# Optimization experiments

Measured on AMD Instinct MI355X. Metric: run time of the kernel, lower is better.

## Reference

```python
import jax, jax.numpy as jnp
import numpy as np

C, IN, OUT = 1024, 256, 256
B, N = 256, 1024

def setup_inputs() -> dict:
    key = jax.random.key(0)
    k1, k2, k3 = jax.random.split(key, 3)
    x = jax.random.normal(k1, (B, N, IN), dtype=jnp.float32)
    indices = jax.random.randint(k2, (B,), 0, C, dtype=jnp.int64)
    # kaiming-uniform-style init for weight table [C, IN, OUT]
    bound = float(np.sqrt(6.0 / IN))
    weight = jax.random.uniform(k3, (C, IN, OUT), dtype=jnp.float32, minval=-bound, maxval=bound)
    bias = jnp.zeros((C, 1, OUT), dtype=jnp.float32)
    return {"x": x, "indices": indices, "weight": weight, "bias": bias}

def reference(x, indices, weight, bias):
    # gather per-batch weight tiles, then batched matmul + bias
    w = weight[indices]          # [B, IN, OUT]
    b = bias[indices]            # [B, 1, OUT]
    return jnp.einsum('bni,bio->bno', x, w) + b
```

## Files before the change

kernel.cpp:

```cpp
#include <hip/hip_runtime.h>
#include <cstdint>

#define C_   1024
#define IN_  256
#define OUT_ 256
#define B_   256
#define N_   1024

#define BM 128
#define BK 32
#define NTHREADS 512

typedef __attribute__((ext_vector_type(8))) short short8;
typedef __attribute__((ext_vector_type(4))) float f32x4;

__device__ __forceinline__ uint16_t f2bf(float f) {
    uint32_t u = __builtin_bit_cast(uint32_t, f);
    return (uint16_t)((u + 0x7FFFu + ((u >> 16) & 1u)) >> 16);
}

__device__ __forceinline__ void glds16(const void* g, void* l) {
    __builtin_amdgcn_global_load_lds(
        (const __attribute__((address_space(1))) void*)g,
        (__attribute__((address_space(3))) void*)l,
        16, 0, 0);
}

__global__ __launch_bounds__(256) void prep_wt(
    const float* __restrict__ weight, const int* __restrict__ idx,
    uint16_t* __restrict__ wt) {
    __shared__ float tile[IN_][33];
    const int b  = blockIdx.y;
    const int o0 = blockIdx.x * 32;
    const int ci = idx[b];
    const float* wsrc = weight + (size_t)ci * (IN_ * OUT_);
    const int t = threadIdx.x;

    const int o_l   = t & 31;
    const int kbase = t >> 5;
    #pragma unroll
    for (int rep = 0; rep < 32; ++rep) {
        int k = rep * 8 + kbase;
        tile[k][o_l] = wsrc[k * OUT_ + o0 + o_l];
    }
    __syncthreads();

    const int k2   = (t & 127) * 2;
    const int osel = t >> 7;
    uint32_t* dst = (uint32_t*)(wt + (size_t)b * (IN_ * OUT_));
    #pragma unroll
    for (int rep = 0; rep < 16; ++rep) {
        int o = rep * 2 + osel;
        uint32_t lo = f2bf(tile[k2][o]);
        uint32_t hi = f2bf(tile[k2 + 1][o]);
        dst[((o0 + o) * IN_ + k2) >> 1] = lo | (hi << 16);
    }
}

__global__ __launch_bounds__(NTHREADS, 2) void gemm_bn256(
    const float* __restrict__ x, const int* __restrict__ idx,
    const uint16_t* __restrict__ wt, const float* __restrict__ bias,
    float* __restrict__ out) {
    __shared__ __align__(16) uint8_t smem[32768];
    uint16_t* As = (uint16_t*)smem;
    uint16_t* Ws = (uint16_t*)(smem + 8192);
    float*    Ep = (float*)smem;

    const int b    = blockIdx.y;
    const int n0   = blockIdx.x * BM;
    const int t    = threadIdx.x;
    const int lane = t & 63;
    const int wv   = t >> 6;
    const int wm   = wv >> 2;
    const int wn   = wv & 3;
    const int m    = lane & 15;
    const int g    = lane >> 4;

    const float*    xsrc = x  + (size_t)b * (N_ * IN_) + (size_t)n0 * IN_;
    const uint16_t* wsrc = wt + (size_t)b * (IN_ * OUT_);

    const int arow = t >> 2, aq = t & 3;
    const float* aptr = xsrc + arow * IN_ + aq * 8;

    float4 ra0, ra1;
    auto loadA = [&](int k0) {
        ra0 = *(const float4*)(aptr + k0);
        ra1 = *(const float4*)(aptr + k0 + 4);
    };

    f32x4 acc[4][4] = {};

    loadA(0);
    #pragma unroll
    for (int kt = 0; kt < IN_ / BK; ++kt) {
        const int k0 = kt * BK;
        __syncthreads();

        {
            float af[8] = {ra0.x, ra0.y, ra0.z, ra0.w,
                           ra1.x, ra1.y, ra1.z, ra1.w};
            union { uint16_t u[8]; uint4 v; } pk;
            #pragma unroll
            for (int i = 0; i < 8; ++i) pk.u[i] = f2bf(af[i]);
            *(uint4*)&As[arow * BK + aq * 8] = pk.v;
        }
        #pragma unroll
        for (int j = 0; j < 2; ++j) {
            const uint16_t* gp = wsrc + (size_t)(j * 128 + (t >> 2)) * IN_
                                 + k0 + (t & 3) * 8;
            void* lp = (uint8_t*)Ws + j * 8192 + wv * 1024;
            glds16(gp, lp);
        }
        __syncthreads();

        if (kt < IN_ / BK - 1) loadA(k0 + BK);

        short8 a[4], bb[4];
        #pragma unroll
        for (int mi = 0; mi < 4; ++mi)
            a[mi] = *(const short8*)&As[(wm * 64 + mi * 16 + m) * BK + g * 8];
        #pragma unroll
        for (int ni = 0; ni < 4; ++ni)
            bb[ni] = *(const short8*)&Ws[(wn * 64 + ni * 16 + m) * BK + g * 8];
        #pragma unroll
        for (int mi = 0; mi < 4; ++mi)
            #pragma unroll
            for (int ni = 0; ni < 4; ++ni)
                acc[mi][ni] = __builtin_amdgcn_mfma_f32_16x16x32_bf16(
                    a[mi], bb[ni], acc[mi][ni], 0, 0, 0);
    }

    const int ci = idx[b];
    float bv[4];
    #pragma unroll
    for (int ni = 0; ni < 4; ++ni)
        bv[ni] = bias[(size_t)ci * OUT_ + wn * 64 + ni * 16 + m];

    float* odst = out + (size_t)b * (N_ * OUT_) + (size_t)n0 * OUT_;
    const int rd_row = t >> 4;
    const int c4b    = t & 15;
    #pragma unroll
    for (int mi = 0; mi < 4; ++mi) {
        __syncthreads();
        #pragma unroll
        for (int ni = 0; ni < 4; ++ni)
            #pragma unroll
            for (int v = 0; v < 4; ++v)
                Ep[(wm * 16 + g * 4 + v) * OUT_ + wn * 64 + ni * 16 + m] =
                    acc[mi][ni][v] + bv[ni];
        __syncthreads();
        const int orow = (rd_row >> 4) * 64 + mi * 16 + (rd_row & 15);
        const float4* ep4 = (const float4*)Ep;
        float4* o4 = (float4*)(odst + orow * OUT_);
        #pragma unroll
        for (int rep = 0; rep < 4; ++rep) {
            int c4 = rep * 16 + c4b;
            o4[c4] = ep4[rd_row * 64 + c4];
        }
    }
}

extern "C" void kernel_launch(void* const* d_in, const int* in_sizes, int n_in,
                              void* d_out, int out_size, void* d_ws, size_t ws_size,
                              hipStream_t stream) {
    const float* x      = (const float*)d_in[0];
    const int*   idx    = (const int*)d_in[1];
    const float* weight = (const float*)d_in[2];
    const float* bias   = (const float*)d_in[3];
    float*       out    = (float*)d_out;
    uint16_t*    wt     = (uint16_t*)d_ws;

    prep_wt<<<dim3(8, B_), 256, 0, stream>>>(weight, idx, wt);
    gemm_bn256<<<dim3(N_ / BM, B_), NTHREADS, 0, stream>>>(x, idx, wt, bias, out);
}
```

Baseline: 595.1 us.

## Fuse weight prep into GEMM with register-resident bf16 weight fragments per batch

Removes the separate weight transpose/convert kernel and its workspace round trip. Each block now handles a whole batch: it stages the gathered fp32 weight through LDS, converts it to bf16 MFMA fragments held in registers, then loops over all 1024 rows of x with double-buffered A tiles and writes output directly without an LDS epilogue. This cuts grid parallelism to 256 blocks and raises register pressure, and the direct output stores are less coalesced.

```diff
diff --git a/kernel.cpp b/kernel.cpp
--- a/kernel.cpp
+++ b/kernel.cpp
@@ -7,9 +7,8 @@
 #define B_   256
 #define N_   1024
 
-#define BM 128
-#define BK 32
 #define NTHREADS 512
+#define WLD 260
 
 typedef __attribute__((ext_vector_type(8))) short short8;
 typedef __attribute__((ext_vector_type(4))) float f32x4;
@@ -19,144 +18,121 @@
     return (uint16_t)((u + 0x7FFFu + ((u >> 16) & 1u)) >> 16);
 }
 
-__device__ __forceinline__ void glds16(const void* g, void* l) {
-    __builtin_amdgcn_global_load_lds(
-        (const __attribute__((address_space(1))) void*)g,
-        (__attribute__((address_space(3))) void*)l,
-        16, 0, 0);
-}
+__global__ __launch_bounds__(NTHREADS, 2) void fused_gemm(
+    const float* __restrict__ x, const int* __restrict__ idx,
+    const float* __restrict__ weight, const float* __restrict__ bias,
+    float* __restrict__ out) {
+    __shared__ __align__(16) uint8_t smem[WLD * 32 * 4];
+    float*    wstg = (float*)smem;
+    uint16_t* As0  = (uint16_t*)smem;
+    uint16_t* As1  = (uint16_t*)(smem + 8192);
 
-__global__ __launch_bounds__(256) void prep_wt(
-    const float* __restrict__ weight, const int* __restrict__ idx,
-    uint16_t* __restrict__ wt) {
-    __shared__ float tile[IN_][33];
-    const int b  = blockIdx.y;
-    const int o0 = blockIdx.x * 32;
-    const int ci = idx[b];
-    const float* wsrc = weight + (size_t)ci * (IN_ * OUT_);
-    const int t = threadIdx.x;
-
-    const int o_l   = t & 31;
-    const int kbase = t >> 5;
-    #pragma unroll
-    for (int rep = 0; rep < 32; ++rep) {
-        int k = rep * 8 + kbase;
-        tile[k][o_l] = wsrc[k * OUT_ + o0 + o_l];
-    }
-    __syncthreads();
-
-    const int k2   = (t & 127) * 2;
-    const int osel = t >> 7;
-    uint32_t* dst = (uint32_t*)(wt + (size_t)b * (IN_ * OUT_));
-    #pragma unroll
-    for (int rep = 0; rep < 16; ++rep) {
-        int o = rep * 2 + osel;
-        uint32_t lo = f2bf(tile[k2][o]);
-        uint32_t hi = f2bf(tile[k2 + 1][o]);
-        dst[((o0 + o) * IN_ + k2) >> 1] = lo | (hi << 16);
-    }
-}
-
-__global__ __launch_bounds__(NTHREADS, 2) void gemm_bn256(
-    const float* __restrict__ x, const int* __restrict__ idx,
-    const uint16_t* __restrict__ wt, const float* __restrict__ bias,
-    float* __restrict__ out) {
-    __shared__ __align__(16) uint8_t smem[32768];
-    uint16_t* As = (uint16_t*)smem;
-    uint16_t* Ws = (uint16_t*)(smem + 8192);
-    float*    Ep = (float*)smem;
-
-    const int b    = blockIdx.y;
-    const int n0   = blockIdx.x * BM;
+    const int b    = blockIdx.x;
     const int t    = threadIdx.x;
     const int lane = t & 63;
     const int wv   = t >> 6;
-    const int wm   = wv >> 2;
-    const int wn   = wv & 3;
     const int m    = lane & 15;
     const int g    = lane >> 4;
+    const int ci   = idx[b];
 
-    const float*    xsrc = x  + (size_t)b * (N_ * IN_) + (size_t)n0 * IN_;
-    const uint16_t* wsrc = wt + (size_t)b * (IN_ * OUT_);
+    const float* xsrc = x      + (size_t)b  * (N_ * IN_);
+    const float* wsrc = weight + (size_t)ci * (IN_ * OUT_);
+    float*       odst = out    + (size_t)b  * (N_ * OUT_);
 
     const int arow = t >> 2, aq = t & 3;
-    const float* aptr = xsrc + arow * IN_ + aq * 8;
+    const float* abase = xsrc + arow * IN_ + aq * 8;
+    float4 xe0 = *(const float4*)(abase);
+    float4 xe1 = *(const float4*)(abase + 4);
+    float4 xo0 = *(const float4*)(abase + 32);
+    float4 xo1 = *(const float4*)(abase + 36);
 
-    float4 ra0, ra1;
-    auto loadA = [&](int k0) {
-        ra0 = *(const float4*)(aptr + k0);
-        ra1 = *(const float4*)(aptr + k0 + 4);
-    };
-
-    f32x4 acc[4][4] = {};
-
-    loadA(0);
+    short8 bb[8][2];
+    const int wrow = t >> 6;
+    const int wc   = (t & 63) * 4;
+    const float* wbase = wsrc + wrow * OUT_ + wc;
+    float4 wA[4], wB[4];
     #pragma unroll
-    for (int kt = 0; kt < IN_ / BK; ++kt) {
-        const int k0 = kt * BK;
+    for (int r = 0; r < 4; ++r)
+        wA[r] = *(const float4*)(wbase + (r * 8) * OUT_);
+    #pragma unroll
+    for (int kc = 0; kc < 8; ++kc) {
+        float4* wr = (kc & 1) ? wB : wA;
+        #pragma unroll
+        for (int r = 0; r < 4; ++r)
+            *(float4*)(wstg + (r * 8 + wrow) * WLD + wc) = wr[r];
         __syncthreads();
-
-        {
-            float af[8] = {ra0.x, ra0.y, ra0.z, ra0.w,
-                           ra1.x, ra1.y, ra1.z, ra1.w};
-            union { uint16_t u[8]; uint4 v; } pk;
+        if (kc < 7) {
+            float4* wnx = (kc & 1) ? wA : wB;
             #pragma unroll
-            for (int i = 0; i < 8; ++i) pk.u[i] = f2bf(af[i]);
-            *(uint4*)&As[arow * BK + aq * 8] = pk.v;
+            for (int r = 0; r < 4; ++r)
+                wnx[r] = *(const float4*)(wbase + ((kc + 1) * 32 + r * 8) * OUT_);
         }
         #pragma unroll
-        for (int j = 0; j < 2; ++j) {
-            const uint16_t* gp = wsrc + (size_t)(j * 128 + (t >> 2)) * IN_
-                                 + k0 + (t & 3) * 8;
-            void* lp = (uint8_t*)Ws + j * 8192 + wv * 1024;
-            glds16(gp, lp);
+        for (int ni = 0; ni < 2; ++ni) {
+            const int o = wv * 32 + ni * 16 + m;
+            short8 f;
+            #pragma unroll
+            for (int j = 0; j < 8; ++j)
+                f[j] = (short)f2bf(wstg[(g * 8 + j) * WLD + o]);
+            bb[kc][ni] = f;
         }
         __syncthreads();
-
-        if (kt < IN_ / BK - 1) loadA(k0 + BK);
-
-        short8 a[4], bb[4];
-        #pragma unroll
-        for (int mi = 0; mi < 4; ++mi)
-            a[mi] = *(const short8*)&As[(wm * 64 + mi * 16 + m) * BK + g * 8];
-        #pragma unroll
-        for (int ni = 0; ni < 4; ++ni)
-            bb[ni] = *(const short8*)&Ws[(wn * 64 + ni * 16 + m) * BK + g * 8];
-        #pragma unroll
-        for (int mi = 0; mi < 4; ++mi)
-            #pragma unroll
-            for (int ni = 0; ni < 4; ++ni)
-                acc[mi][ni] = __builtin_amdgcn_mfma_f32_16x16x32_bf16(
-                    a[mi], bb[ni], acc[mi][ni], 0, 0, 0);
     }
 
-    const int ci = idx[b];
-    float bv[4];
+    float bv[2];
     #pragma unroll
-    for (int ni = 0; ni < 4; ++ni)
-        bv[ni] = bias[(size_t)ci * OUT_ + wn * 64 + ni * 16 + m];
+    for (int ni = 0; ni < 2; ++ni)
+        bv[ni] = bias[(size_t)ci * OUT_ + wv * 32 + ni * 16 + m];
 
-    float* odst = out + (size_t)b * (N_ * OUT_) + (size_t)n0 * OUT_;
-    const int rd_row = t >> 4;
-    const int c4b    = t & 15;
-    #pragma unroll
-    for (int mi = 0; mi < 4; ++mi) {
-        __syncthreads();
+    f32x4 acc[8][2] = {};
+    for (int nt = 0; nt < 8; ++nt) {
         #pragma unroll
-        for (int ni = 0; ni < 4; ++ni)
+        for (int kt = 0; kt < 8; ++kt) {
+            uint16_t* Asb = (kt & 1) ? As1 : As0;
+            float4 c0 = (kt & 1) ? xo0 : xe0;
+            float4 c1 = (kt & 1) ? xo1 : xe1;
+            {
+                float af[8] = {c0.x, c0.y, c0.z, c0.w,
+                               c1.x, c1.y, c1.z, c1.w};
+                union { uint16_t u[8]; uint4 v; } pk;
+                #pragma unroll
+                for (int i = 0; i < 8; ++i) pk.u[i] = f2bf(af[i]);
+                *(uint4*)&Asb[arow * 32 + aq * 8] = pk.v;
+            }
+            {
+                const int s2 = nt * 8 + kt + 2;
+                if (s2 < 64) {
+                    const float* p = xsrc + ((s2 >> 3) * 128 + arow) * IN_
+                                     + (s2 & 7) * 32 + aq * 8;
+                    float4 n0 = *(const float4*)(p);
+                    float4 n1 = *(const float4*)(p + 4);
+                    if (kt & 1) { xo0 = n0; xo1 = n1; }
+                    else        { xe0 = n0; xe1 = n1; }
+                }
+            }
+            __syncthreads();
+            short8 a[8];
             #pragma unroll
-            for (int v = 0; v < 4; ++v)
-                Ep[(wm * 16 + g * 4 + v) * OUT_ + wn * 64 + ni * 16 + m] =
-                    acc[mi][ni][v] + bv[ni];
-        __syncthreads();
-        const int orow = (rd_row >> 4) * 64 + mi * 16 + (rd_row & 15);
-        const float4* ep4 = (const float4*)Ep;
-        float4* o4 = (float4*)(odst + orow * OUT_);
+            for (int mi = 0; mi < 8; ++mi)
+                a[mi] = *(const short8*)&Asb[(mi * 16 + m) * 32 + g * 8];
+            #pragma unroll
+            for (int mi = 0; mi < 8; ++mi)
+                #pragma unroll
+                for (int ni = 0; ni < 2; ++ni)
+                    acc[mi][ni] = __builtin_amdgcn_mfma_f32_16x16x32_bf16(
+                        a[mi], bb[kt][ni], acc[mi][ni], 0, 0, 0);
+        }
+        float* obase = odst + (size_t)(nt * 128) * OUT_;
         #pragma unroll
-        for (int rep = 0; rep < 4; ++rep) {
-            int c4 = rep * 16 + c4b;
-            o4[c4] = ep4[rd_row * 64 + c4];
-        }
+        for (int mi = 0; mi < 8; ++mi)
+            #pragma unroll
+            for (int ni = 0; ni < 2; ++ni) {
+                #pragma unroll
+                for (int v = 0; v < 4; ++v)
+                    obase[(mi * 16 + g * 4 + v) * OUT_ + wv * 32 + ni * 16 + m]
+                        = acc[mi][ni][v] + bv[ni];
+                acc[mi][ni] = (f32x4){0.f, 0.f, 0.f, 0.f};
+            }
     }
 }
 
@@ -168,8 +144,7 @@
     const float* weight = (const float*)d_in[2];
     const float* bias   = (const float*)d_in[3];
     float*       out    = (float*)d_out;
-    uint16_t*    wt     = (uint16_t*)d_ws;
+    (void)d_ws; (void)ws_size;
 
-    prep_wt<<<dim3(8, B_), 256, 0, stream>>>(weight, idx, wt);
-    gemm_bn256<<<dim3(N_ / BM, B_), NTHREADS, 0, stream>>>(x, idx, wt, bias, out);
+    fused_gemm<<<dim3(B_), NTHREADS, 0, stream>>>(x, idx, weight, bias, out);
 }
```

Result: no change. 594.0 us (-0.2%).
